# Optimization experiments

Measured on AMD Instinct MI355X. Metric: run time of the kernel, lower is better.

## Reference

```python
import jax, jax.numpy as jnp
import numpy as np

N_HEADS = 8
NS = 4  # samples per point


def _ref_grid(H, W):
    # matches torch: pts[i,j] = ((i+0.5)/(H-1), (j+0.5)/(W-1)) * 2 - 1  -> (y, x)
    ys = ((jnp.arange(H, dtype=jnp.float32) + 0.5) / (H - 1)) * 2.0 - 1.0
    xs = ((jnp.arange(W, dtype=jnp.float32) + 0.5) / (W - 1)) * 2.0 - 1.0
    ref = jnp.stack(jnp.meshgrid(ys, xs, indexing='ij'), axis=-1)  # [H,W,2]
    return ref.reshape(H * W, 2)


def _bilinear_sample(img_flat, yx, H, W):
    # img_flat: [D, H*W], yx: [L, n, 2] normalized (y,x) in [-1,1]
    # grid_sample(mode='bilinear', padding_mode='zeros', align_corners=True)
    y = (yx[..., 0] + 1.0) * 0.5 * (H - 1)
    x = (yx[..., 1] + 1.0) * 0.5 * (W - 1)
    y0 = jnp.floor(y)
    x0 = jnp.floor(x)
    out = jnp.zeros((img_flat.shape[0],) + y.shape, dtype=img_flat.dtype)
    for dy in (0.0, 1.0):
        for dx in (0.0, 1.0):
            yi = y0 + dy
            xi = x0 + dx
            w = (1.0 - jnp.abs(y - yi)) * (1.0 - jnp.abs(x - xi))
            valid = (yi >= 0) & (yi < H) & (xi >= 0) & (xi < W)
            yc = jnp.clip(yi, 0, H - 1).astype(jnp.int32)
            xc = jnp.clip(xi, 0, W - 1).astype(jnp.int32)
            idx = yc * W + xc  # [L,n]
            vals = jnp.take(img_flat, idx.reshape(-1), axis=1).reshape(
                img_flat.shape[0], *idx.shape)  # [D,L,n]
            out = out + vals * jnp.where(valid, w, 0.0)[None]
    return out  # [D,L,n]


def setup_inputs() -> dict:
    key = jax.random.key(0)
    ks = jax.random.split(key, 9)
    B, C, H, W = 8, 256, 64, 64
    A, N = N_HEADS, NS
    x = jax.random.normal(ks[0], (B, C, H, W), dtype=jnp.float32)
    w_att = jax.random.normal(ks[1], (A * N, C), dtype=jnp.float32) * 0.02
    b_att = jnp.zeros((A * N,), dtype=jnp.float32)
    w_off = jax.random.normal(ks[2], (A * N * 2, C), dtype=jnp.float32) * 0.01
    b_off = jax.random.normal(ks[3], (A * N * 2,), dtype=jnp.float32) * 0.1
    w_v = jax.random.normal(ks[4], (C, C), dtype=jnp.float32) * 0.02
    b_v = jnp.zeros((C,), dtype=jnp.float32)
    w_out = jax.random.normal(ks[5], (C, C), dtype=jnp.float32) * 0.02
    b_out = jnp.zeros((C,), dtype=jnp.float32)
    return {"x": x, "w_att": w_att, "b_att": b_att, "w_off": w_off,
            "b_off": b_off, "w_v": w_v, "b_v": b_v, "w_out": w_out,
            "b_out": b_out}


def reference(x, w_att, b_att, w_off, b_off, w_v, b_v, w_out, b_out):
    B, C, H, W = x.shape
    A, N = N_HEADS, NS
    D = C // A
    L = H * W
    xl = x.reshape(B, C, L).transpose(0, 2, 1)  # [B,L,C]
    attn = jax.nn.softmax((xl @ w_att.T + b_att).reshape(B, L, A, N), axis=-1)
    off = (xl @ w_off.T + b_off).reshape(B, L, A, N, 2)
    ref = _ref_grid(H, W)  # [L,2] (y,x)
    pos = ref[None, :, None, None, :] + off  # [B,L,A,N,2]
    pos = pos.transpose(0, 2, 1, 3, 4).reshape(B * A, L, N, 2)
    v = jnp.einsum('bchw,oc->bohw', x, w_v) + b_v[None, :, None, None]
    v_flat = v.reshape(B * A, D, L)
    samp = jax.vmap(lambda im, g: _bilinear_sample(im, g, H, W))(v_flat, pos)  # [BA,D,L,N]
    attn_ = attn.transpose(0, 2, 1, 3).reshape(B * A, L, N)
    agg = (samp * attn_[:, None]).sum(axis=3)  # [BA,D,L]
    v2 = agg.reshape(B, A * D, H, W)
    y = jnp.einsum('bchw,oc->bohw', v2, w_out) + b_out[None, :, None, None]
    return y
```

## Files before the change

### kernel.cpp

```cpp
#include <hip/hip_runtime.h>
#include <math.h>
#include <stdint.h>

#define BQ 8
#define CC 256
#define HH 64
#define WW 64
#define LL 4096
#define AH 8
#define DD 32

typedef __attribute__((ext_vector_type(4))) float f32x4;
typedef __attribute__((ext_vector_type(8))) short short8;

__device__ __forceinline__ uint32_t pk_bf16(float a, float b) {
    uint32_t r;
    asm("v_cvt_pk_bf16_f32 %0, %1, %2" : "=v"(r) : "v"(a), "v"(b));
    return r;
}
__device__ __forceinline__ float bf_lo(uint32_t u) { return __uint_as_float(u << 16); }
__device__ __forceinline__ float bf_hi(uint32_t u) { return __uint_as_float(u & 0xffff0000u); }

__device__ __forceinline__ void split2(float a, float b, uint32_t& hi, uint32_t& lo) {
    hi = pk_bf16(a, b);
    float ah = bf_lo(hi), bh = bf_hi(hi);
    lo = pk_bf16(a - ah, b - bh);
}


__device__ __forceinline__ void load8(float4 v[8], const float* p, size_t stride) {
#pragma unroll
    for (int i = 0; i < 8; ++i) v[i] = *(const float4*)(p + (size_t)i * stride);
}

__device__ __forceinline__ void writeA(const float4 av[8], uint32_t* as, int a_r0, int a_f4) {
#pragma unroll
    for (int i = 0; i < 8; ++i) {
        int r = a_r0 + i * 16;
        uint32_t lo = pk_bf16(av[i].x, av[i].y);
        uint32_t hi = pk_bf16(av[i].z, av[i].w);
        int slot = (a_f4 >> 1) ^ (r & 7);
        *(uint2*)&as[r * 32 + (slot << 2) + ((a_f4 & 1) << 1)] = make_uint2(lo, hi);
    }
}

__device__ __forceinline__ void writeB_x(const float4 bv[8], uint32_t* bs, int b_kb, int b_l0) {
#pragma unroll
    for (int j = 0; j < 4; ++j) {
        int l = b_l0 * 4 + j;
        uint32_t w0 = pk_bf16(((const float*)&bv[0])[j], ((const float*)&bv[1])[j]);
        uint32_t w1 = pk_bf16(((const float*)&bv[2])[j], ((const float*)&bv[3])[j]);
        uint32_t w2 = pk_bf16(((const float*)&bv[4])[j], ((const float*)&bv[5])[j]);
        uint32_t w3 = pk_bf16(((const float*)&bv[6])[j], ((const float*)&bv[7])[j]);
        int slot = b_kb ^ (l & 7);
        *(uint4*)&bs[l * 32 + (slot << 2)] = make_uint4(w0, w1, w2, w3);
    }
}

__device__ __forceinline__ void compute_tile(const uint32_t* as, const uint32_t* bs,
                                             f32x4 acc[4][4], int lane, int wm, int wn) {
#pragma unroll
    for (int ks = 0; ks < 2; ++ks) {
        int ag = ks * 4 + (lane >> 4);
        short8 af[4], bf[4];
#pragma unroll
        for (int mf = 0; mf < 4; ++mf) {
            int r = wm * 64 + mf * 16 + (lane & 15);
            af[mf] = *(const short8*)&as[r * 32 + ((ag ^ (r & 7)) << 2)];
        }
#pragma unroll
        for (int nf = 0; nf < 4; ++nf) {
            int r = wn * 64 + nf * 16 + (lane & 15);
            bf[nf] = *(const short8*)&bs[r * 32 + ((ag ^ (r & 7)) << 2)];
        }
#pragma unroll
        for (int mf = 0; mf < 4; ++mf)
#pragma unroll
            for (int nf = 0; nf < 4; ++nf)
                acc[mf][nf] = __builtin_amdgcn_mfma_f32_16x16x32_bf16(
                    af[mf], bf[nf], acc[mf][nf], 0, 0, 0);
    }
}

__global__ __launch_bounds__(256, 2)
void gemm_attoff(const float* __restrict__ X,
                 const float* __restrict__ w_att, const float* __restrict__ w_off,
                 const float* __restrict__ b_att, const float* __restrict__ b_off,
                 float* __restrict__ outbuf)
{
    __shared__ uint32_t ah_s[2][96 * 32];
    __shared__ uint32_t al_s[2][96 * 32];
    __shared__ uint32_t bh_s[2][64 * 32];
    __shared__ uint32_t bl_s[2][64 * 32];

    const int lb = blockIdx.x;
    const int b  = blockIdx.y;
    const int t  = threadIdx.x;
    const int lane = t & 63;
    const int wv = t >> 6;
    const int wm = wv >> 1, wn = wv & 1;

    const int tr   = t >> 4;
    const int a_f4 = t & 15;
    const int b_kb = t & 7;
    const int b_l0 = t >> 3;

    const float* Bp = X + ((size_t)b * CC + b_kb * 8) * LL + lb * 64 + b_l0 * 2;

    f32x4 acc[3][2];
#pragma unroll
    for (int i = 0; i < 3; ++i)
#pragma unroll
        for (int j = 0; j < 2; ++j) acc[i][j] = (f32x4)0.0f;

    float4 av[6];
    float2 bv[8];

    auto loadT = [&](int kc) {
#pragma unroll
        for (int i = 0; i < 6; ++i) {
            int r = i * 16 + tr;
            const float* wp = (i < 2) ? (w_att + (size_t)r * CC)
                                      : (w_off + (size_t)(r - 32) * CC);
            av[i] = *(const float4*)(wp + kc * 64 + a_f4 * 4);
        }
#pragma unroll
        for (int m = 0; m < 8; ++m)
            bv[m] = *(const float2*)(Bp + (size_t)(kc * 64 + m) * LL);
    };

    auto writeT = [&](int buf) {
#pragma unroll
        for (int i = 0; i < 6; ++i) {
            int r = i * 16 + tr;
            uint32_t h0, q0, h1, q1;
            split2(av[i].x, av[i].y, h0, q0);
            split2(av[i].z, av[i].w, h1, q1);
            int idx = r * 32 + (((a_f4 >> 1) ^ (r & 7)) << 2) + ((a_f4 & 1) << 1);
            *(uint2*)&ah_s[buf][idx] = make_uint2(h0, h1);
            *(uint2*)&al_s[buf][idx] = make_uint2(q0, q1);
        }
#pragma unroll
        for (int j = 0; j < 2; ++j) {
            int l = b_l0 * 2 + j;
            uint32_t h[4], q[4];
#pragma unroll
            for (int p = 0; p < 4; ++p) {
                float e0 = j ? bv[2 * p].y     : bv[2 * p].x;
                float e1 = j ? bv[2 * p + 1].y : bv[2 * p + 1].x;
                split2(e0, e1, h[p], q[p]);
            }
            int idx = l * 32 + ((b_kb ^ (l & 7)) << 2);
            *(uint4*)&bh_s[buf][idx] = make_uint4(h[0], h[1], h[2], h[3]);
            *(uint4*)&bl_s[buf][idx] = make_uint4(q[0], q[1], q[2], q[3]);
        }
    };

    auto computeT = [&](int buf) {
#pragma unroll
        for (int ks = 0; ks < 2; ++ks) {
            int ag = ks * 4 + (lane >> 4);
            short8 afh[3], afl[3], bfh[2], bfl[2];
#pragma unroll
            for (int mf = 0; mf < 3; ++mf) {
                int r = wm * 48 + mf * 16 + (lane & 15);
                int off = r * 32 + ((ag ^ (r & 7)) << 2);
                afh[mf] = *(const short8*)&ah_s[buf][off];
                afl[mf] = *(const short8*)&al_s[buf][off];
            }
#pragma unroll
            for (int nf = 0; nf < 2; ++nf) {
                int r = wn * 32 + nf * 16 + (lane & 15);
                int off = r * 32 + ((ag ^ (r & 7)) << 2);
                bfh[nf] = *(const short8*)&bh_s[buf][off];
                bfl[nf] = *(const short8*)&bl_s[buf][off];
            }
#pragma unroll
            for (int mf = 0; mf < 3; ++mf)
#pragma unroll
                for (int nf = 0; nf < 2; ++nf) {
                    acc[mf][nf] = __builtin_amdgcn_mfma_f32_16x16x32_bf16(
                        afh[mf], bfh[nf], acc[mf][nf], 0, 0, 0);
                    acc[mf][nf] = __builtin_amdgcn_mfma_f32_16x16x32_bf16(
                        afh[mf], bfl[nf], acc[mf][nf], 0, 0, 0);
                    acc[mf][nf] = __builtin_amdgcn_mfma_f32_16x16x32_bf16(
                        afl[mf], bfh[nf], acc[mf][nf], 0, 0, 0);
                }
        }
    };

    loadT(0);
    writeT(0);
    __syncthreads();
    for (int kc = 0; kc < 4; ++kc) {
        const int cur = kc & 1;
        if (kc < 3) loadT(kc + 1);
        computeT(cur);
        if (kc < 3) { writeT(cur ^ 1); __syncthreads(); }
    }

    const int l_base = lb * 64 + wn * 32 + (lane & 15);
    const int o_base = wm * 48 + ((lane >> 4) << 2);
#pragma unroll
    for (int mf = 0; mf < 3; ++mf) {
        int o0 = o_base + mf * 16;
        const float* bp = (o0 < 32) ? (b_att + o0) : (b_off + (o0 - 32));
        float4 bs = *(const float4*)bp;
#pragma unroll
        for (int nf = 0; nf < 2; ++nf) {
            int l = l_base + nf * 16;
            float* op = outbuf + ((size_t)b * 96 + o0) * LL + l;
            op[(size_t)0 * LL] = acc[mf][nf][0] + bs.x;
            op[(size_t)1 * LL] = acc[mf][nf][1] + bs.y;
            op[(size_t)2 * LL] = acc[mf][nf][2] + bs.z;
            op[(size_t)3 * LL] = acc[mf][nf][3] + bs.w;
        }
    }
}

__global__ __launch_bounds__(256, 2)
void gemm_v(const float* __restrict__ X, const float* __restrict__ Wm,
            const float* __restrict__ bias, uint16_t* __restrict__ vout)
{
    __shared__ uint32_t a_s[2][128 * 32];
    __shared__ uint32_t b_s[2][128 * 32];

    const int nb = blockIdx.x;
    const int b  = nb >> 5;
    const int lb = nb & 31;
    const int ob = blockIdx.y;
    const int t  = threadIdx.x;
    const int lane = t & 63;
    const int wv = t >> 6;
    const int wm = wv >> 1, wn = wv & 1;

    const int a_f4 = t & 15, a_r0 = t >> 4;
    const int b_kb = t & 7,  b_l0 = t >> 3;

    const float* Ap = Wm + (size_t)(ob * 128 + a_r0) * CC + a_f4 * 4;
    const float* Bp = X + ((size_t)b * CC + b_kb * 8) * LL + lb * 128 + b_l0 * 4;

    f32x4 acc[4][4];
#pragma unroll
    for (int i = 0; i < 4; ++i)
#pragma unroll
        for (int j = 0; j < 4; ++j) acc[i][j] = (f32x4)0.0f;

    float4 av[8], bv[8];
    load8(av, Ap, (size_t)16 * CC);
    load8(bv, Bp, (size_t)LL);
    writeA(av, a_s[0], a_r0, a_f4);
    writeB_x(bv, b_s[0], b_kb, b_l0);
    __syncthreads();

    for (int kc = 0; kc < 4; ++kc) {
        const int cur = kc & 1;
        if (kc < 3) {
            load8(av, Ap + (kc + 1) * 64, (size_t)16 * CC);
            load8(bv, Bp + (size_t)(kc + 1) * 64 * LL, (size_t)LL);
        }
        compute_tile(a_s[cur], b_s[cur], acc, lane, wm, wn);
        if (kc < 3) {
            writeA(av, a_s[cur ^ 1], a_r0, a_f4);
            writeB_x(bv, b_s[cur ^ 1], b_kb, b_l0);
            __syncthreads();
        }
    }

    const int l_base = lb * 128 + wn * 64 + (lane & 15);
    const int o_base = ob * 128 + wm * 64 + ((lane >> 4) << 2);
#pragma unroll
    for (int mf = 0; mf < 4; ++mf) {
        int o0 = o_base + mf * 16;
        float4 bs = *(const float4*)(bias + o0);
        int a_h = o0 >> 5;
        int d0 = o0 & 31;
#pragma unroll
        for (int nf = 0; nf < 4; ++nf) {
            int l = l_base + nf * 16;
            uint32_t p0 = pk_bf16(acc[mf][nf][0] + bs.x, acc[mf][nf][1] + bs.y);
            uint32_t p1 = pk_bf16(acc[mf][nf][2] + bs.z, acc[mf][nf][3] + bs.w);
            *(uint2*)(vout + ((size_t)(b * AH + a_h) * LL + l) * DD + d0) =
                make_uint2(p0, p1);
        }
    }
}

__global__ __launch_bounds__(256, 2)
void gemm_out(const uint16_t* __restrict__ Agg, const float* __restrict__ Wm,
              const float* __restrict__ bias, float* __restrict__ out)
{
    __shared__ uint32_t a_s[2][128 * 32];
    __shared__ uint32_t b_s[2][128 * 32];

    const int nb = blockIdx.x;
    const int b  = nb >> 5;
    const int lb = nb & 31;
    const int ob = blockIdx.y;
    const int t  = threadIdx.x;
    const int lane = t & 63;
    const int wv = t >> 6;
    const int wm = wv >> 1, wn = wv & 1;

    const int a_f4 = t & 15, a_r0 = t >> 4;
    const int br = t >> 1;
    const int bh = t & 1;

    const float* Ap = Wm + (size_t)(ob * 128 + a_r0) * CC + a_f4 * 4;
    const uint16_t* Bp = Agg + ((size_t)b * LL + lb * 128 + br) * CC + bh * 32;

    f32x4 acc[4][4];
#pragma unroll
    for (int i = 0; i < 4; ++i)
#pragma unroll
        for (int j = 0; j < 4; ++j) acc[i][j] = (f32x4)0.0f;

    float4 av[8];
    uint4 bq[4];
    load8(av, Ap, (size_t)16 * CC);
#pragma unroll
    for (int j = 0; j < 4; ++j) bq[j] = *(const uint4*)(Bp + j * 8);
    writeA(av, a_s[0], a_r0, a_f4);
#pragma unroll
    for (int j = 0; j < 4; ++j)
        *(uint4*)&b_s[0][br * 32 + ((((bh << 2) + j) ^ (br & 7)) << 2)] = bq[j];
    __syncthreads();

    for (int kc = 0; kc < 4; ++kc) {
        const int cur = kc & 1;
        if (kc < 3) {
            load8(av, Ap + (kc + 1) * 64, (size_t)16 * CC);
#pragma unroll
            for (int j = 0; j < 4; ++j)
                bq[j] = *(const uint4*)(Bp + (kc + 1) * 64 + j * 8);
        }
        compute_tile(a_s[cur], b_s[cur], acc, lane, wm, wn);
        if (kc < 3) {
            writeA(av, a_s[cur ^ 1], a_r0, a_f4);
#pragma unroll
            for (int j = 0; j < 4; ++j)
                *(uint4*)&b_s[cur ^ 1][br * 32 + ((((bh << 2) + j) ^ (br & 7)) << 2)] = bq[j];
            __syncthreads();
        }
    }

    const int l_base = lb * 128 + wn * 64 + (lane & 15);
    const int o_base = ob * 128 + wm * 64 + ((lane >> 4) << 2);
#pragma unroll
    for (int mf = 0; mf < 4; ++mf) {
        int o0 = o_base + mf * 16;
        float4 bs = *(const float4*)(bias + o0);
#pragma unroll
        for (int nf = 0; nf < 4; ++nf) {
            int l = l_base + nf * 16;
            float* op = out + ((size_t)b * CC + o0) * LL + l;
            op[(size_t)0 * LL] = acc[mf][nf][0] + bs.x;
            op[(size_t)1 * LL] = acc[mf][nf][1] + bs.y;
            op[(size_t)2 * LL] = acc[mf][nf][2] + bs.z;
            op[(size_t)3 * LL] = acc[mf][nf][3] + bs.w;
        }
    }
}

__global__ __launch_bounds__(256)
void sample_kernel(const uint16_t* __restrict__ v_samp,
                   const float* __restrict__ logits,
                   uint16_t* __restrict__ agg)
{
    const int bid  = blockIdx.x;
    const int xcd  = bid & 7;
    const int rest = bid >> 3;
    const int img  = rest >> 6;
    const int lt   = rest & 63;
    const int ba   = xcd * 8 + img;
    const int b = ba >> 3, a = ba & 7;

    const int t  = threadIdx.x;
    const int l  = lt * 64 + (t >> 2);
    const int d0 = (t & 3) * 8;

    const float* la = logits + ((size_t)b * 96 + a * 4) * LL + l;
    float e0 = la[0], e1 = la[(size_t)LL], e2 = la[(size_t)2 * LL], e3 = la[(size_t)3 * LL];
    float m = fmaxf(fmaxf(e0, e1), fmaxf(e2, e3));
    e0 = expf(e0 - m); e1 = expf(e1 - m); e2 = expf(e2 - m); e3 = expf(e3 - m);
    float inv = 1.0f / (e0 + e1 + e2 + e3);
    float attn[4] = {e0 * inv, e1 * inv, e2 * inv, e3 * inv};

    const int gi = l >> 6, gj = l & 63;
    float ry = (gi + 0.5f) * (2.0f / 63.0f) - 1.0f;
    float rx = (gj + 0.5f) * (2.0f / 63.0f) - 1.0f;
    const float* lo = logits + ((size_t)b * 96 + 32 + a * 8) * LL + l;
    float pyy[4], pxx[4];
#pragma unroll
    for (int n = 0; n < 4; ++n) {
        pyy[n] = ry + lo[(size_t)(n * 2 + 0) * LL];
        pxx[n] = rx + lo[(size_t)(n * 2 + 1) * LL];
    }

    float acc[8];
#pragma unroll
    for (int q = 0; q < 8; ++q) acc[q] = 0.f;

    const uint16_t* vb = v_samp + (size_t)ba * LL * DD + d0;
#pragma unroll
    for (int n = 0; n < 4; ++n) {
        float y = (pyy[n] + 1.0f) * 0.5f * 63.0f;
        float x = (pxx[n] + 1.0f) * 0.5f * 63.0f;
        float yf = floorf(y), xf = floorf(x);
        int y0i = (int)yf, x0i = (int)xf;
        float fy = y - yf, fx = x - xf;
        float wts[4] = {(1.f - fy) * (1.f - fx), (1.f - fy) * fx,
                        fy * (1.f - fx),         fy * fx};
        int yy[4] = {y0i, y0i, y0i + 1, y0i + 1};
        int xx[4] = {x0i, x0i + 1, x0i, x0i + 1};
#pragma unroll
        for (int c2 = 0; c2 < 4; ++c2) {
            int yc = yy[c2], xc = xx[c2];
            if (yc >= 0 && yc < HH && xc >= 0 && xc < WW) {
                float w = attn[n] * wts[c2];
                uint4 rv = *(const uint4*)(vb + (size_t)(yc * WW + xc) * DD);
                acc[0] += w * bf_lo(rv.x); acc[1] += w * bf_hi(rv.x);
                acc[2] += w * bf_lo(rv.y); acc[3] += w * bf_hi(rv.y);
                acc[4] += w * bf_lo(rv.z); acc[5] += w * bf_hi(rv.z);
                acc[6] += w * bf_lo(rv.w); acc[7] += w * bf_hi(rv.w);
            }
        }
    }
    uint32_t p0 = pk_bf16(acc[0], acc[1]);
    uint32_t p1 = pk_bf16(acc[2], acc[3]);
    uint32_t p2 = pk_bf16(acc[4], acc[5]);
    uint32_t p3 = pk_bf16(acc[6], acc[7]);
    *(uint4*)(agg + ((size_t)b * LL + l) * CC + a * DD + d0) =
        make_uint4(p0, p1, p2, p3);
}

extern "C" void kernel_launch(void* const* d_in, const int* in_sizes, int n_in,
                              void* d_out, int out_size, void* d_ws, size_t ws_size,
                              hipStream_t stream) {
    const float* x     = (const float*)d_in[0];
    const float* w_att = (const float*)d_in[1];
    const float* b_att = (const float*)d_in[2];
    const float* w_off = (const float*)d_in[3];
    const float* b_off = (const float*)d_in[4];
    const float* w_v   = (const float*)d_in[5];
    const float* b_v   = (const float*)d_in[6];
    const float* w_out = (const float*)d_in[7];
    const float* b_out = (const float*)d_in[8];
    float* out = (float*)d_out;

    float* ws      = (float*)d_ws;
    float* logits  = ws;
    uint16_t* agg  = (uint16_t*)(logits + (size_t)BQ * 96 * LL);
    uint16_t* v_samp = (uint16_t*)d_out;

    dim3 blk(256);
    gemm_attoff<<<dim3(64, BQ), blk, 0, stream>>>(x, w_att, w_off, b_att, b_off, logits);
    gemm_v<<<dim3(256, 2), blk, 0, stream>>>(x, w_v, b_v, v_samp);
    sample_kernel<<<dim3(4096), blk, 0, stream>>>(v_samp, logits, agg);
    gemm_out<<<dim3(256, 2), blk, 0, stream>>>(agg, w_out, b_out, out);
}
```

Before: 67.14 us.

## Fuse bilinear sampling with output projection GEMM via shared-memory aggregate tile

```diff
diff --git a/kernel.cpp b/kernel.cpp
--- a/kernel.cpp
+++ b/kernel.cpp
@@ -80,6 +80,22 @@
                 acc[mf][nf] = __builtin_amdgcn_mfma_f32_16x16x32_bf16(
                     af[mf], bf[nf], acc[mf][nf], 0, 0, 0);
     }
+}
+
+__global__ __launch_bounds__(256)
+void pack_wout(const float* __restrict__ Wm, uint32_t* __restrict__ w_pack)
+{
+    int id = blockIdx.x * 256 + threadIdx.x;
+    int lane  = id & 63;
+    int kc    = (id >> 6) & 7;
+    int otile = id >> 9;
+    int o  = otile * 16 + (lane & 15);
+    int k0 = kc * 32 + (lane >> 4) * 8;
+    const float* wp = Wm + (size_t)o * CC + k0;
+    float4 v0 = *(const float4*)wp;
+    float4 v1 = *(const float4*)(wp + 4);
+    ((uint4*)w_pack)[id] = make_uint4(pk_bf16(v0.x, v0.y), pk_bf16(v0.z, v0.w),
+                                      pk_bf16(v1.x, v1.y), pk_bf16(v1.z, v1.w));
 }
 
 __global__ __launch_bounds__(256, 2)
@@ -287,151 +303,136 @@
 }
 
 __global__ __launch_bounds__(256, 2)
-void gemm_out(const uint16_t* __restrict__ Agg, const float* __restrict__ Wm,
-              const float* __restrict__ bias, float* __restrict__ out)
+void sample_out(const uint16_t* __restrict__ v_samp,
+                const float* __restrict__ logits,
+                const uint32_t* __restrict__ w_pack,
+                const float* __restrict__ bias,
+                float* __restrict__ out)
 {
-    __shared__ uint32_t a_s[2][128 * 32];
-    __shared__ uint32_t b_s[2][128 * 32];
-
-    const int nb = blockIdx.x;
-    const int b  = nb >> 5;
-    const int lb = nb & 31;
-    const int ob = blockIdx.y;
-    const int t  = threadIdx.x;
+    __shared__ uint32_t agg_s[64 * 128];
+
+    const int bid = blockIdx.x;
+    const int b   = bid & 7;
+    const int lt  = bid >> 3;
+    const int t   = threadIdx.x;
     const int lane = t & 63;
-    const int wv = t >> 6;
-    const int wm = wv >> 1, wn = wv & 1;
-
-    const int a_f4 = t & 15, a_r0 = t >> 4;
-    const int br = t >> 1;
-    const int bh = t & 1;
-
-    const float* Ap = Wm + (size_t)(ob * 128 + a_r0) * CC + a_f4 * 4;
-    const uint16_t* Bp = Agg + ((size_t)b * LL + lb * 128 + br) * CC + bh * 32;
-
-    f32x4 acc[4][4];
+    const int wv  = t >> 6;
+
+    const int l_loc = t & 63;
+    const int l = lt * 64 + l_loc;
+    const int gi = l >> 6, gj = l & 63;
+    const float ry = (gi + 0.5f) * (2.0f / 63.0f) - 1.0f;
+    const float rx = (gj + 0.5f) * (2.0f / 63.0f) - 1.0f;
+
+#pragma unroll
+    for (int hh = 0; hh < 2; ++hh) {
+        const int a = (t >> 6) + hh * 4;
+
+        const float* la = logits + ((size_t)b * 96 + a * 4) * LL + l;
+        float e0 = la[0], e1 = la[(size_t)LL], e2 = la[(size_t)2 * LL], e3 = la[(size_t)3 * LL];
+        float m = fmaxf(fmaxf(e0, e1), fmaxf(e2, e3));
+        e0 = expf(e0 - m); e1 = expf(e1 - m); e2 = expf(e2 - m); e3 = expf(e3 - m);
+        float inv = 1.0f / (e0 + e1 + e2 + e3);
+        float attn[4] = {e0 * inv, e1 * inv, e2 * inv, e3 * inv};
+
+        const float* lo = logits + ((size_t)b * 96 + 32 + a * 8) * LL + l;
+        float pyy[4], pxx[4];
+#pragma unroll
+        for (int n = 0; n < 4; ++n) {
+            pyy[n] = ry + lo[(size_t)(n * 2 + 0) * LL];
+            pxx[n] = rx + lo[(size_t)(n * 2 + 1) * LL];
+        }
+
+        float acc[32];
+#pragma unroll
+        for (int q = 0; q < 32; ++q) acc[q] = 0.f;
+
+        const uint16_t* vb = v_samp + (size_t)(b * AH + a) * LL * DD;
+#pragma unroll
+        for (int n = 0; n < 4; ++n) {
+            float y = (pyy[n] + 1.0f) * 0.5f * 63.0f;
+            float x = (pxx[n] + 1.0f) * 0.5f * 63.0f;
+            float yf = floorf(y), xf = floorf(x);
+            int y0i = (int)yf, x0i = (int)xf;
+            float fy = y - yf, fx = x - xf;
+            float wts[4] = {(1.f - fy) * (1.f - fx), (1.f - fy) * fx,
+                            fy * (1.f - fx),         fy * fx};
+            int yy[4] = {y0i, y0i, y0i + 1, y0i + 1};
+            int xx[4] = {x0i, x0i + 1, x0i, x0i + 1};
+#pragma unroll
+            for (int c2 = 0; c2 < 4; ++c2) {
+                int yc = yy[c2], xc = xx[c2];
+                if (yc >= 0 && yc < HH && xc >= 0 && xc < WW) {
+                    float w = attn[n] * wts[c2];
+                    const uint4* vp = (const uint4*)(vb + (size_t)(yc * WW + xc) * DD);
+#pragma unroll
+                    for (int u = 0; u < 4; ++u) {
+                        uint4 rv = vp[u];
+                        acc[u * 8 + 0] += w * bf_lo(rv.x);
+                        acc[u * 8 + 1] += w * bf_hi(rv.x);
+                        acc[u * 8 + 2] += w * bf_lo(rv.y);
+                        acc[u * 8 + 3] += w * bf_hi(rv.y);
+                        acc[u * 8 + 4] += w * bf_lo(rv.z);
+                        acc[u * 8 + 5] += w * bf_hi(rv.z);
+                        acc[u * 8 + 6] += w * bf_lo(rv.w);
+                        acc[u * 8 + 7] += w * bf_hi(rv.w);
+                    }
+                }
+            }
+        }
+#pragma unroll
+        for (int j = 0; j < 4; ++j) {
+            int slot = (a * 4 + j) ^ (l_loc & 7);
+            uint32_t p0 = pk_bf16(acc[j * 8 + 0], acc[j * 8 + 1]);
+            uint32_t p1 = pk_bf16(acc[j * 8 + 2], acc[j * 8 + 3]);
+            uint32_t p2 = pk_bf16(acc[j * 8 + 4], acc[j * 8 + 5]);
+            uint32_t p3 = pk_bf16(acc[j * 8 + 6], acc[j * 8 + 7]);
+            *(uint4*)&agg_s[l_loc * 128 + (slot << 2)] = make_uint4(p0, p1, p2, p3);
+        }
+    }
+    __syncthreads();
+
+    f32x4 acc2[4][4];
 #pragma unroll
     for (int i = 0; i < 4; ++i)
 #pragma unroll
-        for (int j = 0; j < 4; ++j) acc[i][j] = (f32x4)0.0f;
-
-    float4 av[8];
-    uint4 bq[4];
-    load8(av, Ap, (size_t)16 * CC);
-#pragma unroll
-    for (int j = 0; j < 4; ++j) bq[j] = *(const uint4*)(Bp + j * 8);
-    writeA(av, a_s[0], a_r0, a_f4);
-#pragma unroll
-    for (int j = 0; j < 4; ++j)
-        *(uint4*)&b_s[0][br * 32 + ((((bh << 2) + j) ^ (br & 7)) << 2)] = bq[j];
-    __syncthreads();
-
-    for (int kc = 0; kc < 4; ++kc) {
-        const int cur = kc & 1;
-        if (kc < 3) {
-            load8(av, Ap + (kc + 1) * 64, (size_t)16 * CC);
-#pragma unroll
-            for (int j = 0; j < 4; ++j)
-                bq[j] = *(const uint4*)(Bp + (kc + 1) * 64 + j * 8);
-        }
-        compute_tile(a_s[cur], b_s[cur], acc, lane, wm, wn);
-        if (kc < 3) {
-            writeA(av, a_s[cur ^ 1], a_r0, a_f4);
-#pragma unroll
-            for (int j = 0; j < 4; ++j)
-                *(uint4*)&b_s[cur ^ 1][br * 32 + ((((bh << 2) + j) ^ (br & 7)) << 2)] = bq[j];
-            __syncthreads();
-        }
-    }
-
-    const int l_base = lb * 128 + wn * 64 + (lane & 15);
-    const int o_base = ob * 128 + wm * 64 + ((lane >> 4) << 2);
+        for (int j = 0; j < 4; ++j) acc2[i][j] = (f32x4)0.0f;
+
+    for (int kc = 0; kc < 8; ++kc) {
+        short8 af[4], bf[4];
+#pragma unroll
+        for (int mf = 0; mf < 4; ++mf) {
+            int otile = wv * 4 + mf;
+            af[mf] = *(const short8*)&w_pack[(size_t)((otile * 8 + kc) * 64 + lane) * 4];
+        }
+#pragma unroll
+        for (int nf = 0; nf < 4; ++nf) {
+            int r = nf * 16 + (lane & 15);
+            int slot = kc * 4 + (lane >> 4);
+            bf[nf] = *(const short8*)&agg_s[r * 128 + ((slot ^ (r & 7)) << 2)];
+        }
+#pragma unroll
+        for (int mf = 0; mf < 4; ++mf)
+#pragma unroll
+            for (int nf = 0; nf < 4; ++nf)
+                acc2[mf][nf] = __builtin_amdgcn_mfma_f32_16x16x32_bf16(
+                    af[mf], bf[nf], acc2[mf][nf], 0, 0, 0);
+    }
+
 #pragma unroll
     for (int mf = 0; mf < 4; ++mf) {
-        int o0 = o_base + mf * 16;
+        int o0 = wv * 64 + mf * 16 + ((lane >> 4) << 2);
         float4 bs = *(const float4*)(bias + o0);
 #pragma unroll
         for (int nf = 0; nf < 4; ++nf) {
-            int l = l_base + nf * 16;
-            float* op = out + ((size_t)b * CC + o0) * LL + l;
-            op[(size_t)0 * LL] = acc[mf][nf][0] + bs.x;
-            op[(size_t)1 * LL] = acc[mf][nf][1] + bs.y;
-            op[(size_t)2 * LL] = acc[mf][nf][2] + bs.z;
-            op[(size_t)3 * LL] = acc[mf][nf][3] + bs.w;
-        }
-    }
-}
-
-__global__ __launch_bounds__(256)
-void sample_kernel(const uint16_t* __restrict__ v_samp,
-                   const float* __restrict__ logits,
-                   uint16_t* __restrict__ agg)
-{
-    const int bid  = blockIdx.x;
-    const int xcd  = bid & 7;
-    const int rest = bid >> 3;
-    const int img  = rest >> 6;
-    const int lt   = rest & 63;
-    const int ba   = xcd * 8 + img;
-    const int b = ba >> 3, a = ba & 7;
-
-    const int t  = threadIdx.x;
-    const int l  = lt * 64 + (t >> 2);
-    const int d0 = (t & 3) * 8;
-
-    const float* la = logits + ((size_t)b * 96 + a * 4) * LL + l;
-    float e0 = la[0], e1 = la[(size_t)LL], e2 = la[(size_t)2 * LL], e3 = la[(size_t)3 * LL];
-    float m = fmaxf(fmaxf(e0, e1), fmaxf(e2, e3));
-    e0 = expf(e0 - m); e1 = expf(e1 - m); e2 = expf(e2 - m); e3 = expf(e3 - m);
-    float inv = 1.0f / (e0 + e1 + e2 + e3);
-    float attn[4] = {e0 * inv, e1 * inv, e2 * inv, e3 * inv};
-
-    const int gi = l >> 6, gj = l & 63;
-    float ry = (gi + 0.5f) * (2.0f / 63.0f) - 1.0f;
-    float rx = (gj + 0.5f) * (2.0f / 63.0f) - 1.0f;
-    const float* lo = logits + ((size_t)b * 96 + 32 + a * 8) * LL + l;
-    float pyy[4], pxx[4];
-#pragma unroll
-    for (int n = 0; n < 4; ++n) {
-        pyy[n] = ry + lo[(size_t)(n * 2 + 0) * LL];
-        pxx[n] = rx + lo[(size_t)(n * 2 + 1) * LL];
-    }
-
-    float acc[8];
-#pragma unroll
-    for (int q = 0; q < 8; ++q) acc[q] = 0.f;
-
-    const uint16_t* vb = v_samp + (size_t)ba * LL * DD + d0;
-#pragma unroll
-    for (int n = 0; n < 4; ++n) {
-        float y = (pyy[n] + 1.0f) * 0.5f * 63.0f;
-        float x = (pxx[n] + 1.0f) * 0.5f * 63.0f;
-        float yf = floorf(y), xf = floorf(x);
-        int y0i = (int)yf, x0i = (int)xf;
-        float fy = y - yf, fx = x - xf;
-        float wts[4] = {(1.f - fy) * (1.f - fx), (1.f - fy) * fx,
-                        fy * (1.f - fx),         fy * fx};
-        int yy[4] = {y0i, y0i, y0i + 1, y0i + 1};
-        int xx[4] = {x0i, x0i + 1, x0i, x0i + 1};
-#pragma unroll
-        for (int c2 = 0; c2 < 4; ++c2) {
-            int yc = yy[c2], xc = xx[c2];
-            if (yc >= 0 && yc < HH && xc >= 0 && xc < WW) {
-                float w = attn[n] * wts[c2];
-                uint4 rv = *(const uint4*)(vb + (size_t)(yc * WW + xc) * DD);
-                acc[0] += w * bf_lo(rv.x); acc[1] += w * bf_hi(rv.x);
-                acc[2] += w * bf_lo(rv.y); acc[3] += w * bf_hi(rv.y);
-                acc[4] += w * bf_lo(rv.z); acc[5] += w * bf_hi(rv.z);
-                acc[6] += w * bf_lo(rv.w); acc[7] += w * bf_hi(rv.w);
-            }
-        }
-    }
-    uint32_t p0 = pk_bf16(acc[0], acc[1]);
-    uint32_t p1 = pk_bf16(acc[2], acc[3]);
-    uint32_t p2 = pk_bf16(acc[4], acc[5]);
-    uint32_t p3 = pk_bf16(acc[6], acc[7]);
-    *(uint4*)(agg + ((size_t)b * LL + l) * CC + a * DD + d0) =
-        make_uint4(p0, p1, p2, p3);
+            int lx = lt * 64 + nf * 16 + (lane & 15);
+            float* op = out + ((size_t)b * CC + o0) * LL + lx;
+            op[(size_t)0 * LL] = acc2[mf][nf][0] + bs.x;
+            op[(size_t)1 * LL] = acc2[mf][nf][1] + bs.y;
+            op[(size_t)2 * LL] = acc2[mf][nf][2] + bs.z;
+            op[(size_t)3 * LL] = acc2[mf][nf][3] + bs.w;
+        }
+    }
 }
 
 extern "C" void kernel_launch(void* const* d_in, const int* in_sizes, int n_in,
@@ -448,14 +449,14 @@
     const float* b_out = (const float*)d_in[8];
     float* out = (float*)d_out;
 
-    float* ws      = (float*)d_ws;
-    float* logits  = ws;
-    uint16_t* agg  = (uint16_t*)(logits + (size_t)BQ * 96 * LL);
-    uint16_t* v_samp = (uint16_t*)d_out;
+    float* ws        = (float*)d_ws;
+    float* logits    = ws;
+    uint16_t* v_samp = (uint16_t*)(logits + (size_t)BQ * 96 * LL);
+    uint32_t* w_pack = (uint32_t*)(v_samp + (size_t)BQ * AH * LL * DD);
 
     dim3 blk(256);
+    pack_wout<<<dim3(32), blk, 0, stream>>>(w_out, w_pack);
     gemm_attoff<<<dim3(64, BQ), blk, 0, stream>>>(x, w_att, w_off, b_att, b_off, logits);
     gemm_v<<<dim3(256, 2), blk, 0, stream>>>(x, w_v, b_v, v_samp);
-    sample_kernel<<<dim3(4096), blk, 0, stream>>>(v_samp, logits, agg);
-    gemm_out<<<dim3(256, 2), blk, 0, stream>>>(agg, w_out, b_out, out);
-}
+    sample_out<<<dim3(512), blk, 0, stream>>>(v_samp, logits, w_pack, b_out, out);
+}
```

New measurement: 68.88 us. +2.6%, slower.
